# Kernel tuning notes

Measured on AMD Instinct MI355X. Metric: run time of the kernel, lower is better.

The kernel has to match this reference:

```python
import jax, jax.numpy as jnp
from jax import lax
import numpy as np

N_MTF = 41

def _gaussian2d(N, std):
    t = np.arange(-(N - 1) / 2, (N + 1) / 2)
    t1, t2 = np.meshgrid(t, t)
    return np.exp(-0.5 * (t1 / std) ** 2) * np.exp(-0.5 * (t2 / std) ** 2)

def _kaiser2d(N, beta):
    t = np.arange(-(N - 1) / 2, (N + 1) / 2) / np.double(N - 1)
    t1, t2 = np.meshgrid(t, t)
    t12 = np.sqrt(t1 * t1 + t2 * t2)
    w1 = np.kaiser(N, beta)
    w = np.interp(t12, t, w1)
    w[t12 > t[-1]] = 0
    w[t12 < t[0]] = 0
    return w

def _fir_filter_wind(Hd, w):
    hd = np.rot90(np.fft.fftshift(np.rot90(Hd, 2)), 2)
    h = np.fft.fftshift(np.fft.ifft2(hd))
    h = np.rot90(h, 2)
    return h * w

def gen_mtf_kernels(ratio, nbands):
    GNyq = np.asarray([0.34, 0.32, 0.3, 0.22], dtype='float32')[:nbands]  # QB sensor
    h = np.zeros((nbands, N_MTF, N_MTF), dtype='float32')
    fcut = 1.0 / ratio
    for ii in range(nbands):
        alpha = np.sqrt(((N_MTF - 1) * (fcut / 2)) ** 2 / (-2 * np.log(GNyq[ii])))
        H = _gaussian2d(N_MTF, alpha)
        Hd = H / np.max(H)
        w = _kaiser2d(N_MTF, 0.5)
        h[ii] = np.real(_fir_filter_wind(Hd, w)).astype('float32')
    return h

def gen_interp23_kernel():
    cdf23 = 2.0 * np.array([0.5, 0.305334091185, 0.0, -0.072698593239, 0.0,
                            0.021809577942, 0.0, -0.005192756653, 0.0,
                            0.000807762146, 0.0, -6.0081482e-05])
    d = cdf23[::-1]
    return np.concatenate([d[:-1], cdf23]).astype('float32')  # 23 taps

_DN = ('NCHW', 'OIHW', 'NCHW')

def _sep_filter_circular(img, k):
    # img: (bs, c, H, W); k: (K,) separable kernel, circular padding per torch F.pad('circular')
    bs, c, H, W = img.shape
    P = (k.shape[0] - 1) // 2
    f = img.reshape(bs * c, 1, H, W)
    f = jnp.pad(f, ((0, 0), (0, 0), (0, 0), (P, P)), mode='wrap')
    f = lax.conv_general_dilated(f, k.reshape(1, 1, 1, -1), (1, 1), 'VALID', dimension_numbers=_DN)
    f = jnp.pad(f, ((0, 0), (0, 0), (P, P), (0, 0)), mode='wrap')
    f = lax.conv_general_dilated(f, k.reshape(1, 1, -1, 1), (1, 1), 'VALID', dimension_numbers=_DN)
    return f.reshape(bs, c, H, W)

def interp23tap(x, kernel, num_upsamples):
    cur = x
    for k in range(num_upsamples):
        bs, c, h, w = cur.shape
        up = jnp.zeros((bs, c, 2 * h, 2 * w), cur.dtype)
        if k == 0:
            up = up.at[..., 1::2, 1::2].set(cur)
        else:
            up = up.at[..., ::2, ::2].set(cur)
        cur = _sep_filter_circular(up, kernel)
    return cur

def setup_inputs() -> dict:
    key = jax.random.key(0)
    bs, nbands, H, W = 4, 4, 1024, 1024
    ratio = 4
    x = jax.random.normal(key, (bs, nbands, H, W), dtype=jnp.float32)
    mtf_kernels = jnp.asarray(gen_mtf_kernels(ratio, nbands))          # (nbands, 41, 41)
    interp_kernel = jnp.asarray(gen_interp23_kernel())                  # (23,)
    pan_weights = jnp.full((nbands,), 1.0 / nbands, dtype=jnp.float32)  # 'mean' pan weights
    return {"x": x, "mtf_kernels": mtf_kernels, "interp_kernel": interp_kernel,
            "pan_weights": pan_weights, "ratio": ratio}

def reference(x, mtf_kernels, interp_kernel, pan_weights, ratio):
    # Simulated PAN: spectral weighting of HR bands
    pan = jnp.einsum('bchw,c->bhw', x, pan_weights)[:, None]  # (bs,1,H,W)
    # MTF blur: depthwise 41x41 conv with replicate padding
    nbands = x.shape[1]
    pad = mtf_kernels.shape[-1] // 2
    xp = jnp.pad(x, ((0, 0), (0, 0), (pad, pad), (pad, pad)), mode='edge')
    blurred = lax.conv_general_dilated(xp, mtf_kernels[:, None], (1, 1), 'VALID',
                                       dimension_numbers=_DN, feature_group_count=nbands)
    # Downsample: avgpool with kernel=stride=ratio
    bs, c, H, W = blurred.shape
    lrms = blurred.reshape(bs, c, H // ratio, ratio, W // ratio, ratio).mean(axis=(3, 5))
    # Upsample back via 23-tap polynomial interpolation (ratio = 2**num_upsamples)
    num_ups = int(ratio).bit_length() - 1
    ms_up = interp23tap(lrms, interp_kernel, num_ups)
    return pan, lrms, ms_up
```

## Files before the change

kernel.cpp:

```cpp
#include <hip/hip_runtime.h>

#define PAN_SZ  4194304
#define LRMS_OFF 4194304
#define MS_OFF  5242880

__global__ __launch_bounds__(256) void build_keff_kernel(
    const float* __restrict__ mtf, float* __restrict__ keff) {
  int e = blockIdx.x * 256 + threadIdx.x;
  if (e >= 4 * 44 * 44) return;
  int c = e / 1936;
  int rem = e - c * 1936;
  int p = rem / 44;
  int q = rem - p * 44;
  float s = 0.f;
  for (int di = 0; di < 4; ++di) {
    int u = p - di;
    if (u < 0 || u > 40) continue;
    for (int dj = 0; dj < 4; ++dj) {
      int v = q - dj;
      if (v < 0 || v > 40) continue;
      s += mtf[(c * 41 + u) * 41 + v];
    }
  }
  keff[e] = s * 0.0625f;
}

__global__ __launch_bounds__(256) void pan_kernel(
    const float* __restrict__ x, const float* __restrict__ w,
    float* __restrict__ pan) {
  int g = blockIdx.x * 256 + threadIdx.x;
  int b = g >> 18;
  int e = g & 262143;
  const float4* x4 = (const float4*)x;
  float w0 = w[0], w1 = w[1], w2 = w[2], w3 = w[3];
  float4 a0 = x4[(size_t)(b * 4 + 0) * 262144 + e];
  float4 a1 = x4[(size_t)(b * 4 + 1) * 262144 + e];
  float4 a2 = x4[(size_t)(b * 4 + 2) * 262144 + e];
  float4 a3 = x4[(size_t)(b * 4 + 3) * 262144 + e];
  float4 o;
  o.x = a0.x * w0 + a1.x * w1 + a2.x * w2 + a3.x * w3;
  o.y = a0.y * w0 + a1.y * w1 + a2.y * w2 + a3.y * w3;
  o.z = a0.z * w0 + a1.z * w1 + a2.z * w2 + a3.z * w3;
  o.w = a0.w * w0 + a1.w * w1 + a2.w * w2 + a3.w * w3;
  ((float4*)pan)[g] = o;
}

__global__ __launch_bounds__(256) void lrms_kernel(
    const float* __restrict__ x, const float* __restrict__ keff,
    float* __restrict__ lrms) {
  __shared__ __align__(16) float Ksh[1936];
  __shared__ __align__(16) float P[4][272];

  int img = blockIdx.y;
  int rg  = blockIdx.x;
  int ch  = img & 3;
  int tid = threadIdx.x;

  for (int e = tid; e < 1936; e += 256) Ksh[e] = keff[ch * 1936 + e];

  int c = tid & 63;
  int r = tid >> 6;
  int i0 = rg * 4;
  const float* ximg = x + (size_t)img * 1048576;

  float acc0 = 0.f, acc1 = 0.f, acc2 = 0.f, acc3 = 0.f;
  __syncthreads();

  for (int t = 0; t < 56; ++t) {
    int gy = 4 * i0 + t - 20;
    gy = gy < 0 ? 0 : (gy > 1023 ? 1023 : gy);
    const float* xrow = ximg + (size_t)gy * 1024;
    for (int cl = tid; cl < 1064; cl += 256) {
      int gx = cl - 20;
      gx = gx < 0 ? 0 : (gx > 1023 ? 1023 : gx);
      P[cl & 3][cl >> 2] = xrow[gx];
    }
    __syncthreads();

    int p = t - 4 * r;
    if (p >= 0 && p < 44) {
      p = __builtin_amdgcn_readfirstlane(p);
      float v[4][16];
      #pragma unroll
      for (int rq = 0; rq < 4; ++rq) {
        const float4* ph = (const float4*)(&P[rq][0]);
        #pragma unroll
        for (int j = 0; j < 4; ++j) {
          float4 t4 = ph[c + j];
          v[rq][4 * j + 0] = t4.x;
          v[rq][4 * j + 1] = t4.y;
          v[rq][4 * j + 2] = t4.z;
          v[rq][4 * j + 3] = t4.w;
        }
      }
      const float4* K4 = (const float4*)(&Ksh[p * 44]);
      #pragma unroll
      for (int a = 0; a < 11; ++a) {
        float4 kv = K4[a];
        acc0 += v[0][a] * kv.x + v[1][a] * kv.y + v[2][a] * kv.z + v[3][a] * kv.w;
        acc1 += v[0][a+1] * kv.x + v[1][a+1] * kv.y + v[2][a+1] * kv.z + v[3][a+1] * kv.w;
        acc2 += v[0][a+2] * kv.x + v[1][a+2] * kv.y + v[2][a+2] * kv.z + v[3][a+2] * kv.w;
        acc3 += v[0][a+3] * kv.x + v[1][a+3] * kv.y + v[2][a+3] * kv.z + v[3][a+3] * kv.w;
      }
    }
    __syncthreads();
  }

  float4 res = make_float4(acc0, acc1, acc2, acc3);
  ((float4*)lrms)[(size_t)(img * 256 + i0 + r) * 64 + c] = res;
}

__global__ __launch_bounds__(256) void interp_kernel(
    const float* __restrict__ lrms, const float* __restrict__ ik,
    float* __restrict__ ms) {
  __shared__ float lr[32][33];
  __shared__ float t1[32][44];
  __shared__ float s1[43][44];
  __shared__ float t2[43][64];
  __shared__ float k2[12];

  int img = blockIdx.z;
  int bx = blockIdx.x, by = blockIdx.y;
  int tid = threadIdx.x;

  if (tid < 12) k2[tid] = ik[2 * tid];

  const float* L = lrms + (size_t)img * 65536;
  int ybase = by * 16 - 8, xbase = bx * 16 - 8;
  for (int e = tid; e < 32 * 32; e += 256) {
    int yy = e >> 5, xx = e & 31;
    int gy = (ybase + yy) & 255;
    int gx = (xbase + xx) & 255;
    lr[yy][xx] = L[gy * 256 + gx];
  }
  __syncthreads();

  for (int e = tid; e < 32 * 43; e += 256) {
    int yy = e / 43, cc = e - yy * 43;
    float val;
    if ((cc & 1) == 0) {
      val = lr[yy][(cc >> 1) + 5];
    } else {
      int base = (cc - 5) >> 1;
      float s = 0.f;
      #pragma unroll
      for (int t = 0; t < 12; ++t) s += k2[t] * lr[yy][base + 2 + t];
      val = s;
    }
    t1[yy][cc] = val;
  }
  __syncthreads();

  for (int e = tid; e < 43 * 43; e += 256) {
    int rr = e / 43, cc = e - rr * 43;
    float val;
    if ((rr & 1) == 0) {
      val = t1[(rr >> 1) + 5][cc];
    } else {
      int base = (rr - 5) >> 1;
      float s = 0.f;
      #pragma unroll
      for (int t = 0; t < 12; ++t) s += k2[t] * t1[base + 2 + t][cc];
      val = s;
    }
    s1[rr][cc] = val;
  }
  __syncthreads();

  for (int e = tid; e < 43 * 64; e += 256) {
    int rr = e >> 6, mm = e & 63;
    float val;
    if ((mm & 1) == 0) {
      val = s1[rr][(mm >> 1) + 5];
    } else {
      int base = (mm - 1) >> 1;
      float s = 0.f;
      #pragma unroll
      for (int t = 0; t < 12; ++t) s += k2[t] * s1[rr][base + t];
      val = s;
    }
    t2[rr][mm] = val;
  }
  __syncthreads();

  float* O = ms + (size_t)img * 1048576 + (size_t)(by * 64) * 1024 + bx * 64;
  for (int e = tid; e < 64 * 64; e += 256) {
    int nn = e >> 6, mm = e & 63;
    float val;
    if ((nn & 1) == 0) {
      val = t2[(nn >> 1) + 5][mm];
    } else {
      int base = (nn - 1) >> 1;
      float s = 0.f;
      #pragma unroll
      for (int t = 0; t < 12; ++t) s += k2[t] * t2[base + t][mm];
      val = s;
    }
    O[(size_t)nn * 1024 + mm] = val;
  }
}

extern "C" void kernel_launch(void* const* d_in, const int* in_sizes, int n_in,
                              void* d_out, int out_size, void* d_ws, size_t ws_size,
                              hipStream_t stream) {
  const float* x   = (const float*)d_in[0];
  const float* mtf = (const float*)d_in[1];
  const float* ik  = (const float*)d_in[2];
  const float* pw  = (const float*)d_in[3];
  float* out = (float*)d_out;
  float* keff = (float*)d_ws;

  build_keff_kernel<<<31, 256, 0, stream>>>(mtf, keff);
  pan_kernel<<<4096, 256, 0, stream>>>(x, pw, out);
  lrms_kernel<<<dim3(64, 16), 256, 0, stream>>>(x, keff, out + LRMS_OFF);
  interp_kernel<<<dim3(16, 16, 16), 256, 0, stream>>>(out + LRMS_OFF, ik, out + MS_OFF);
}
```

Measured before the change: 357.1 us.

## Restructure lrms conv: 8 output rows per block, float4 loads, double-buffered staging

Each lrms block now computes 8 low-res output rows instead of 4, with each wave handling two adjacent output rows that share the same staged input rows. Input rows are loaded four at a time (one per wave) with vectorized float4 global loads into registers, then written into a double-buffered shared tile, so the next stage's loads overlap with compute. This cuts redundant input reloads across blocks and the number of barriers per block. In exchange it raises register and LDS use and halves the grid to 512 blocks, which may lower occupancy.

Result: faster. 323.5 us (-9.4%).

```diff
diff --git a/kernel.cpp b/kernel.cpp
--- a/kernel.cpp
+++ b/kernel.cpp
@@ -49,65 +49,122 @@
     const float* __restrict__ x, const float* __restrict__ keff,
     float* __restrict__ lrms) {
   __shared__ __align__(16) float Ksh[1936];
-  __shared__ __align__(16) float P[4][272];
+  __shared__ __align__(16) float P[2][4][4][272];
 
   int img = blockIdx.y;
-  int rg  = blockIdx.x;
   int ch  = img & 3;
+  int i0  = blockIdx.x * 8;
   int tid = threadIdx.x;
+  int w   = tid >> 6;
+  int lane = tid & 63;
 
   for (int e = tid; e < 1936; e += 256) Ksh[e] = keff[ch * 1936 + e];
 
-  int c = tid & 63;
-  int r = tid >> 6;
-  int i0 = rg * 4;
   const float* ximg = x + (size_t)img * 1048576;
-
-  float acc0 = 0.f, acc1 = 0.f, acc2 = 0.f, acc3 = 0.f;
-  __syncthreads();
-
-  for (int t = 0; t < 56; ++t) {
-    int gy = 4 * i0 + t - 20;
+  int gybase = 4 * i0 - 20;
+
+  float accA[4] = {0.f, 0.f, 0.f, 0.f};
+  float accB[4] = {0.f, 0.f, 0.f, 0.f};
+  float4 r[5];
+
+  auto ld4c = [&](const float* row, int g) -> float4 {
+    if ((unsigned)g <= 1020u) return *(const float4*)(row + g);
+    float4 v;
+    v.x = row[min(max(g + 0, 0), 1023)];
+    v.y = row[min(max(g + 1, 0), 1023)];
+    v.z = row[min(max(g + 2, 0), 1023)];
+    v.w = row[min(max(g + 3, 0), 1023)];
+    return v;
+  };
+  auto stage_load = [&](int it) {
+    int gy = gybase + 4 * it + w;
     gy = gy < 0 ? 0 : (gy > 1023 ? 1023 : gy);
     const float* xrow = ximg + (size_t)gy * 1024;
-    for (int cl = tid; cl < 1064; cl += 256) {
-      int gx = cl - 20;
-      gx = gx < 0 ? 0 : (gx > 1023 ? 1023 : gx);
-      P[cl & 3][cl >> 2] = xrow[gx];
-    }
-    __syncthreads();
-
-    int p = t - 4 * r;
-    if (p >= 0 && p < 44) {
-      p = __builtin_amdgcn_readfirstlane(p);
-      float v[4][16];
-      #pragma unroll
-      for (int rq = 0; rq < 4; ++rq) {
-        const float4* ph = (const float4*)(&P[rq][0]);
+    #pragma unroll
+    for (int j = 0; j < 5; ++j) {
+      int kk = lane + 64 * j;
+      if (j < 4 || lane < 10) r[j] = ld4c(xrow, 4 * kk - 20);
+    }
+  };
+  auto stage_write = [&](int buf) {
+    float* B = &P[buf][w][0][0];
+    #pragma unroll
+    for (int j = 0; j < 5; ++j) {
+      int kk = lane + 64 * j;
+      if (j < 4 || lane < 10) {
+        B[0 * 272 + kk] = r[j].x;
+        B[1 * 272 + kk] = r[j].y;
+        B[2 * 272 + kk] = r[j].z;
+        B[3 * 272 + kk] = r[j].w;
+      }
+    }
+  };
+
+  stage_load(0);
+  stage_write(0);
+  __syncthreads();
+
+  for (int it = 0; it < 18; ++it) {
+    int cur = it & 1;
+    if (it < 17) stage_load(it + 1);
+
+    #pragma unroll
+    for (int s = 0; s < 4; ++s) {
+      int trel = 4 * it + s;
+      int pA = trel - 8 * w;
+      int pB = pA - 4;
+      bool vA = (unsigned)pA < 44u;
+      bool vB = (unsigned)pB < 44u;
+      if (vA | vB) {
+        float v[4][16];
         #pragma unroll
-        for (int j = 0; j < 4; ++j) {
-          float4 t4 = ph[c + j];
-          v[rq][4 * j + 0] = t4.x;
-          v[rq][4 * j + 1] = t4.y;
-          v[rq][4 * j + 2] = t4.z;
-          v[rq][4 * j + 3] = t4.w;
+        for (int ph = 0; ph < 4; ++ph) {
+          const float4* F = (const float4*)&P[cur][s][ph][0];
+          #pragma unroll
+          for (int j = 0; j < 4; ++j) {
+            float4 t4 = F[lane + j];
+            v[ph][4 * j + 0] = t4.x;
+            v[ph][4 * j + 1] = t4.y;
+            v[ph][4 * j + 2] = t4.z;
+            v[ph][4 * j + 3] = t4.w;
+          }
+        }
+        if (vA) {
+          const float4* K4 = (const float4*)(&Ksh[pA * 44]);
+          #pragma unroll
+          for (int a = 0; a < 11; ++a) {
+            float4 kv = K4[a];
+            #pragma unroll
+            for (int j = 0; j < 4; ++j)
+              accA[j] += v[0][a + j] * kv.x + v[1][a + j] * kv.y +
+                         v[2][a + j] * kv.z + v[3][a + j] * kv.w;
+          }
+        }
+        if (vB) {
+          const float4* K4 = (const float4*)(&Ksh[pB * 44]);
+          #pragma unroll
+          for (int a = 0; a < 11; ++a) {
+            float4 kv = K4[a];
+            #pragma unroll
+            for (int j = 0; j < 4; ++j)
+              accB[j] += v[0][a + j] * kv.x + v[1][a + j] * kv.y +
+                         v[2][a + j] * kv.z + v[3][a + j] * kv.w;
+          }
         }
       }
-      const float4* K4 = (const float4*)(&Ksh[p * 44]);
-      #pragma unroll
-      for (int a = 0; a < 11; ++a) {
-        float4 kv = K4[a];
-        acc0 += v[0][a] * kv.x + v[1][a] * kv.y + v[2][a] * kv.z + v[3][a] * kv.w;
-        acc1 += v[0][a+1] * kv.x + v[1][a+1] * kv.y + v[2][a+1] * kv.z + v[3][a+1] * kv.w;
-        acc2 += v[0][a+2] * kv.x + v[1][a+2] * kv.y + v[2][a+2] * kv.z + v[3][a+2] * kv.w;
-        acc3 += v[0][a+3] * kv.x + v[1][a+3] * kv.y + v[2][a+3] * kv.z + v[3][a+3] * kv.w;
-      }
     }
     __syncthreads();
-  }
-
-  float4 res = make_float4(acc0, acc1, acc2, acc3);
-  ((float4*)lrms)[(size_t)(img * 256 + i0 + r) * 64 + c] = res;
+    if (it < 17) {
+      stage_write(cur ^ 1);
+      __syncthreads();
+    }
+  }
+
+  int oyA = i0 + 2 * w;
+  ((float4*)lrms)[((size_t)img * 256 + oyA) * 64 + lane] =
+      make_float4(accA[0], accA[1], accA[2], accA[3]);
+  ((float4*)lrms)[((size_t)img * 256 + oyA + 1) * 64 + lane] =
+      make_float4(accB[0], accB[1], accB[2], accB[3]);
 }
 
 __global__ __launch_bounds__(256) void interp_kernel(
@@ -212,6 +269,6 @@
 
   build_keff_kernel<<<31, 256, 0, stream>>>(mtf, keff);
   pan_kernel<<<4096, 256, 0, stream>>>(x, pw, out);
-  lrms_kernel<<<dim3(64, 16), 256, 0, stream>>>(x, keff, out + LRMS_OFF);
+  lrms_kernel<<<dim3(32, 16), 256, 0, stream>>>(x, keff, out + LRMS_OFF);
   interp_kernel<<<dim3(16, 16, 16), 256, 0, stream>>>(out + LRMS_OFF, ik, out + MS_OFF);
 }
```

## Restructure lrms conv to register-resident rows with 8 outputs per thread

Applied to the files above, without the earlier changes.

The lrms conv kernel drops the shared-memory row staging and its per-row barriers. Each thread now reads its 44-wide input span straight from global memory as float4s into registers, double-buffered across rows. It accumulates 8 output rows, and each input row is reused across up to 8 kernel-row offsets. Kernel weights are read via uniform (scalar) global loads instead of LDS. This removes syncs and LDS traffic, but it raises register pressure and halves the block count to 512, which may reduce occupancy.

New measurement: 341.5 us. 4.4% less time.

```diff
diff --git a/kernel.cpp b/kernel.cpp
--- a/kernel.cpp
+++ b/kernel.cpp
@@ -48,66 +48,75 @@
 __global__ __launch_bounds__(256) void lrms_kernel(
     const float* __restrict__ x, const float* __restrict__ keff,
     float* __restrict__ lrms) {
-  __shared__ __align__(16) float Ksh[1936];
-  __shared__ __align__(16) float P[4][272];
-
   int img = blockIdx.y;
-  int rg  = blockIdx.x;
   int ch  = img & 3;
-  int tid = threadIdx.x;
-
-  for (int e = tid; e < 1936; e += 256) Ksh[e] = keff[ch * 1936 + e];
-
-  int c = tid & 63;
-  int r = tid >> 6;
-  int i0 = rg * 4;
+  int i0  = blockIdx.x * 8;
+  int oc  = threadIdx.x;
+
   const float* ximg = x + (size_t)img * 1048576;
-
-  float acc0 = 0.f, acc1 = 0.f, acc2 = 0.f, acc3 = 0.f;
-  __syncthreads();
-
-  for (int t = 0; t < 56; ++t) {
-    int gy = 4 * i0 + t - 20;
+  const float* Kc   = keff + ch * 1936;
+
+  float acc[8] = {0.f, 0.f, 0.f, 0.f, 0.f, 0.f, 0.f, 0.f};
+  int c4base = oc - 5;
+  bool interior = (oc >= 5) && (oc <= 250);
+
+  float4 va[11], vb[11];
+
+  auto loadrow = [&](int tt, float4* v) {
+    int gy = 4 * i0 - 20 + tt;
     gy = gy < 0 ? 0 : (gy > 1023 ? 1023 : gy);
-    const float* xrow = ximg + (size_t)gy * 1024;
-    for (int cl = tid; cl < 1064; cl += 256) {
-      int gx = cl - 20;
-      gx = gx < 0 ? 0 : (gx > 1023 ? 1023 : gx);
-      P[cl & 3][cl >> 2] = xrow[gx];
-    }
-    __syncthreads();
-
-    int p = t - 4 * r;
-    if (p >= 0 && p < 44) {
-      p = __builtin_amdgcn_readfirstlane(p);
-      float v[4][16];
-      #pragma unroll
-      for (int rq = 0; rq < 4; ++rq) {
-        const float4* ph = (const float4*)(&P[rq][0]);
-        #pragma unroll
-        for (int j = 0; j < 4; ++j) {
-          float4 t4 = ph[c + j];
-          v[rq][4 * j + 0] = t4.x;
-          v[rq][4 * j + 1] = t4.y;
-          v[rq][4 * j + 2] = t4.z;
-          v[rq][4 * j + 3] = t4.w;
+    const float4* row4 = (const float4*)(ximg + (size_t)gy * 1024);
+    if (interior) {
+      #pragma unroll
+      for (int a = 0; a < 11; ++a) v[a] = row4[c4base + a];
+    } else {
+      const float* rowf = (const float*)row4;
+      #pragma unroll
+      for (int a = 0; a < 11; ++a) {
+        int c4 = c4base + a;
+        if ((unsigned)c4 <= 255u) {
+          v[a] = row4[c4];
+        } else {
+          float4 t;
+          t.x = rowf[min(max(4 * c4 + 0, 0), 1023)];
+          t.y = rowf[min(max(4 * c4 + 1, 0), 1023)];
+          t.z = rowf[min(max(4 * c4 + 2, 0), 1023)];
+          t.w = rowf[min(max(4 * c4 + 3, 0), 1023)];
+          v[a] = t;
         }
       }
-      const float4* K4 = (const float4*)(&Ksh[p * 44]);
-      #pragma unroll
-      for (int a = 0; a < 11; ++a) {
-        float4 kv = K4[a];
-        acc0 += v[0][a] * kv.x + v[1][a] * kv.y + v[2][a] * kv.z + v[3][a] * kv.w;
-        acc1 += v[0][a+1] * kv.x + v[1][a+1] * kv.y + v[2][a+1] * kv.z + v[3][a+1] * kv.w;
-        acc2 += v[0][a+2] * kv.x + v[1][a+2] * kv.y + v[2][a+2] * kv.z + v[3][a+2] * kv.w;
-        acc3 += v[0][a+3] * kv.x + v[1][a+3] * kv.y + v[2][a+3] * kv.z + v[3][a+3] * kv.w;
+    }
+  };
+
+  auto compute = [&](int tt, const float4* v) {
+    #pragma unroll
+    for (int r = 0; r < 8; ++r) {
+      int p = tt - 4 * r;
+      if ((unsigned)p < 44u) {
+        const float* Kr = Kc + __builtin_amdgcn_readfirstlane(p * 44);
+        float s = acc[r];
+        #pragma unroll
+        for (int a = 0; a < 11; ++a) {
+          s += v[a].x * Kr[4 * a + 0] + v[a].y * Kr[4 * a + 1] +
+               v[a].z * Kr[4 * a + 2] + v[a].w * Kr[4 * a + 3];
+        }
+        acc[r] = s;
       }
     }
-    __syncthreads();
-  }
-
-  float4 res = make_float4(acc0, acc1, acc2, acc3);
-  ((float4*)lrms)[(size_t)(img * 256 + i0 + r) * 64 + c] = res;
+  };
+
+  loadrow(0, va);
+  for (int it = 0; it < 36; ++it) {
+    int tt = 2 * it;
+    loadrow(tt + 1, vb);
+    compute(tt, va);
+    if (tt + 2 < 72) loadrow(tt + 2, va);
+    compute(tt + 1, vb);
+  }
+
+  #pragma unroll
+  for (int r = 0; r < 8; ++r)
+    lrms[((size_t)img * 256 + i0 + r) * 256 + oc] = acc[r];
 }
 
 __global__ __launch_bounds__(256) void interp_kernel(
@@ -212,6 +221,6 @@
 
   build_keff_kernel<<<31, 256, 0, stream>>>(mtf, keff);
   pan_kernel<<<4096, 256, 0, stream>>>(x, pw, out);
-  lrms_kernel<<<dim3(64, 16), 256, 0, stream>>>(x, keff, out + LRMS_OFF);
+  lrms_kernel<<<dim3(32, 16), 256, 0, stream>>>(x, keff, out + LRMS_OFF);
   interp_kernel<<<dim3(16, 16, 16), 256, 0, stream>>>(out + LRMS_OFF, ik, out + MS_OFF);
 }
```
